# Performance work log

Hardware: AMD Instinct MI355X
Metric: run time of the kernel (lower is better)

## Reference

```python
import jax, jax.numpy as jnp
import numpy as np

N_ENT, E, M, STEPS, B, H, C = 500000, 128, 8, 3, 4096, 256, 16

def setup_inputs() -> dict:
    key = jax.random.key(0)
    ks = jax.random.split(key, 13)
    s = 0.05
    return {
        "entity_ids": jax.random.randint(ks[0], (B, STEPS + 1), 0, N_ENT),
        "module_ids": jax.random.randint(ks[1], (B, STEPS), 0, M),
        "embedding": jax.random.normal(ks[2], (N_ENT, E), jnp.float32),
        "W_in": jax.random.normal(ks[3], (M, E, E), jnp.float32) * s,
        "b_in": jax.random.normal(ks[4], (M, E), jnp.float32) * s,
        "W_bias": jax.random.normal(ks[5], (M, E, E), jnp.float32) * s,
        "b_bias": jax.random.normal(ks[6], (M, E), jnp.float32) * s,
        "W_f": jax.random.normal(ks[7], (M, 2 * E, E), jnp.float32) * s,
        "b_f": jax.random.normal(ks[8], (M, E), jnp.float32) * s,
        "W1": jax.random.normal(ks[9], (E, H), jnp.float32) * s,
        "b1": jax.random.normal(ks[10], (H,), jnp.float32) * s,
        "W2": jax.random.normal(ks[11], (H, C), jnp.float32) * s,
        "b2": jax.random.normal(ks[12], (C,), jnp.float32) * s,
    }

def reference(entity_ids, module_ids, embedding, W_in, b_in, W_bias, b_bias,
              W_f, b_f, W1, b1, W2, b2):
    # x: [B, E] embedding of each path's start entity
    x = embedding[entity_ids[:, 0]]

    def step(x, inputs):
        mid, eid = inputs                      # [B], [B]
        bias = embedding[eid]                  # [B, E]
        h_in = jax.nn.relu(jnp.einsum('be,beo->bo', x, W_in[mid]) + b_in[mid])
        h_bi = jax.nn.relu(jnp.einsum('be,beo->bo', bias, W_bias[mid]) + b_bias[mid])
        h = jnp.concatenate([h_in, h_bi], axis=1)  # [B, 2E]
        x_new = jnp.tanh(jnp.einsum('bf,bfo->bo', h, W_f[mid]) + b_f[mid])
        return x_new, None

    xs = (module_ids.T, entity_ids[:, 1:].T)   # [STEPS, B] each
    x, _ = jax.lax.scan(step, x, xs)

    # classifier: Linear -> ReLU -> Linear
    h = jax.nn.relu(x @ W1 + b1)
    return h @ W2 + b2
```

## Files before the change

### kernel.cpp

```cpp
#include <hip/hip_runtime.h>

#define BB      4096
#define EE      128
#define MM      8
#define NSTEPS  3
#define HH      256
#define CC      16

#define TS      16
#define NBMAX   (BB/TS + MM)
#define HT      17
#define FB      1024

#define NFRAGBLK 1096

typedef __attribute__((ext_vector_type(8))) short  bf16x8;
typedef __attribute__((ext_vector_type(4))) float  f32x4;

__device__ __forceinline__ unsigned short bf16_rn(float v) {
    unsigned u = __float_as_uint(v);
    return (unsigned short)((u + 0x7FFFu + ((u >> 16) & 1u)) >> 16);
}
__device__ __forceinline__ float bf16_f(unsigned short h) {
    return __uint_as_float(((unsigned)h) << 16);
}
__device__ __forceinline__ void split8(const float* v, bf16x8& hi, bf16x8& lo) {
    #pragma unroll
    for (int i = 0; i < 8; i++) {
        unsigned short h = bf16_rn(v[i]);
        hi[i] = (short)h;
        lo[i] = (short)bf16_rn(v[i] - bf16_f(h));
    }
}
#define MFMA(a,b,c) __builtin_amdgcn_mfma_f32_16x16x32_bf16((a),(b),(c),0,0,0)
__device__ __forceinline__ f32x4 mfma3(bf16x8 ah, bf16x8 al, bf16x8 bh, bf16x8 bl, f32x4 c) {
    c = MFMA(ah, bh, c);
    c = MFMA(ah, bl, c);
    c = MFMA(al, bh, c);
    return c;
}

__global__ __launch_bounds__(256) void convert_kernel(
    const float* __restrict__ W_in, const float* __restrict__ W_bias,
    const float* __restrict__ W_f,  const float* __restrict__ W1,
    const float* __restrict__ W2,   unsigned short* __restrict__ wf)
{
    const int b = blockIdx.x, tid = threadIdx.x;
    unsigned short* dhi = wf + (size_t)b * FB;
    unsigned short* dlo = dhi + 512;
    #pragma unroll
    for (int half = 0; half < 2; half++) {
        const int el = tid + half * 256;
        const int ln = el >> 3, j = el & 7;
        const int krel = ((ln >> 4) << 3) + j;
        const int nrel = ln & 15;
        float v;
        if (b < 512) {
            const int bb = b & 255;
            const int kc = bb & 3, nt = (bb >> 2) & 7, m = bb >> 5;
            const float* src = (b < 256 ? W_in : W_bias) + (size_t)m * EE * EE;
            v = src[(size_t)(kc*32 + krel) * EE + nt*16 + nrel];
        } else if (b < 1024) {
            const int bb = b - 512;
            const int kc = bb & 7, nt = (bb >> 3) & 7, m = bb >> 6;
            v = W_f[(size_t)m * 2*EE*EE + (size_t)(kc*32 + krel) * EE + nt*16 + nrel];
        } else if (b < 1088) {
            const int bb = b - 1024;
            const int kc = bb & 3, nt = bb >> 2;
            v = W1[(size_t)(kc*32 + krel) * HH + nt*16 + nrel];
        } else {
            const int kc = b - 1088;
            v = W2[(size_t)(kc*32 + krel) * CC + nrel];
        }
        const unsigned short h = bf16_rn(v);
        dhi[el] = h;
        dlo[el] = bf16_rn(v - bf16_f(h));
    }
}

__global__ __launch_bounds__(1024) void prep_kernel(
    const int* __restrict__ module_ids,
    int* __restrict__ blockMod,
    int* __restrict__ perm)
{
    __shared__ int waveCnt [16][NSTEPS][MM];
    __shared__ int waveBase[16][NSTEPS][MM];
    __shared__ int cursor  [16][NSTEPS][MM];
    __shared__ int base        [NSTEPS][MM];
    const int tid  = threadIdx.x;
    const int wid  = tid >> 6;
    const int lane = tid & 63;

    if (tid < 16*NSTEPS*MM) (&waveCnt[0][0][0])[tid] = 0;
    for (int i = tid; i < NSTEPS*NBMAX*TS; i += 1024) perm[i] = -1;
    __syncthreads();

    for (int t = 0; t < NSTEPS; t++) {
        #pragma unroll
        for (int c = 0; c < 4; c++) {
            const int s = (wid << 8) + (c << 6) + lane;
            const int m = module_ids[s*NSTEPS + t];
            unsigned long long bal[MM];
            #pragma unroll
            for (int k = 0; k < MM; k++) bal[k] = __ballot(m == k);
            if (lane < MM) waveCnt[wid][t][lane] += __popcll(bal[lane]);
        }
    }
    __syncthreads();

    if (tid < NSTEPS) {
        const int t = tid;
        int blk = 0;
        for (int m = 0; m < MM; m++) {
            int tot = 0;
            for (int w = 0; w < 16; w++) { waveBase[w][t][m] = tot; tot += waveCnt[w][t][m]; }
            base[t][m] = blk * TS;
            const int nb = (tot + TS - 1) / TS;
            for (int b = 0; b < nb; b++) blockMod[t*NBMAX + blk + b] = m;
            blk += nb;
        }
        for (; blk < NBMAX; blk++) blockMod[t*NBMAX + blk] = -1;
    }
    __syncthreads();

    if (tid < 16*NSTEPS*MM) {
        const int w = tid / (NSTEPS*MM), r = tid % (NSTEPS*MM), t = r / MM, m = r % MM;
        cursor[w][t][m] = base[t][m] + waveBase[w][t][m];
    }
    __syncthreads();

    for (int t = 0; t < NSTEPS; t++) {
        #pragma unroll
        for (int c = 0; c < 4; c++) {
            const int s = (wid << 8) + (c << 6) + lane;
            const int m = module_ids[s*NSTEPS + t];
            unsigned long long bal[MM];
            #pragma unroll
            for (int k = 0; k < MM; k++) bal[k] = __ballot(m == k);
            const unsigned long long below = (1ull << lane) - 1ull;
            const int rank = __popcll(bal[m] & below);
            perm[t*NBMAX*TS + cursor[wid][t][m] + rank] = s;
            if (lane < MM) cursor[wid][t][lane] += __popcll(bal[lane]);
        }
    }
}

__global__ __launch_bounds__(256) void step_kernel(
    const int t,
    const int*   __restrict__ entity_ids,
    const float* __restrict__ embedding,
    const float* __restrict__ b_in, const float* __restrict__ b_bias,
    const float* __restrict__ b_f,
    const unsigned short* __restrict__ wf,
    const int*   __restrict__ blockMod,
    const int*   __restrict__ perm,
    float* __restrict__ xbuf)
{
    const int bid = blockIdx.x;
    const int m = blockMod[t*NBMAX + bid];
    if (m < 0) return;
    const int tid  = threadIdx.x;
    const int lane = tid & 63, wave = tid >> 6;
    const int row16 = lane & 15, quad = lane >> 4;
    const int pb = (t*NBMAX + bid)*TS;

    __shared__ float hs[2*EE][HT];

    const int sA = perm[pb + row16];
    int sSt[4];
    #pragma unroll
    for (int r = 0; r < 4; r++) sSt[r] = perm[pb + quad*4 + r];
    const int sAc = sA < 0 ? 0 : sA;

    const float* xrow;
    if (t == 0) {
        const int e0 = entity_ids[sAc*(NSTEPS+1)];
        xrow = embedding + (size_t)e0*EE;
    } else {
        xrow = xbuf + (size_t)sAc*EE;
    }
    const int e1 = entity_ids[sAc*(NSTEPS+1) + t + 1];
    const float* brow = embedding + (size_t)e1*EE;

    bf16x8 xh[4], xl[4], eh[4], el_[4];
    #pragma unroll
    for (int kc = 0; kc < 4; kc++) {
        const int off = kc*32 + quad*8;
        float vv[8];
        *(float4*)(vv)     = *(const float4*)(xrow + off);
        *(float4*)(vv + 4) = *(const float4*)(xrow + off + 4);
        split8(vv, xh[kc], xl[kc]);
        *(float4*)(vv)     = *(const float4*)(brow + off);
        *(float4*)(vv + 4) = *(const float4*)(brow + off + 4);
        split8(vv, eh[kc], el_[kc]);
    }

    f32x4 aci[2] = {{0.f,0.f,0.f,0.f},{0.f,0.f,0.f,0.f}};
    f32x4 acb[2] = {{0.f,0.f,0.f,0.f},{0.f,0.f,0.f,0.f}};
    #pragma unroll
    for (int i = 0; i < 2; i++) {
        const int nt = wave + 4*i;
        #pragma unroll
        for (int kc = 0; kc < 4; kc++) {
            const unsigned short* bI = wf + (size_t)((m*8 + nt)*4 + kc)*FB;
            const unsigned short* bB = wf + (size_t)(256 + (m*8 + nt)*4 + kc)*FB;
            const bf16x8 wih = *(const bf16x8*)(bI + lane*8);
            const bf16x8 wil = *(const bf16x8*)(bI + 512 + lane*8);
            const bf16x8 wbh = *(const bf16x8*)(bB + lane*8);
            const bf16x8 wbl = *(const bf16x8*)(bB + 512 + lane*8);
            aci[i] = mfma3(xh[kc], xl[kc], wih, wil, aci[i]);
            acb[i] = mfma3(eh[kc], el_[kc], wbh, wbl, acb[i]);
        }
    }

    #pragma unroll
    for (int i = 0; i < 2; i++) {
        const int col = (wave + 4*i)*16 + row16;
        const float bin = b_in [m*EE + col];
        const float bbi = b_bias[m*EE + col];
        #pragma unroll
        for (int r = 0; r < 4; r++) {
            hs[col][quad*4 + r]      = fmaxf(aci[i][r] + bin, 0.f);
            hs[EE + col][quad*4 + r] = fmaxf(acb[i][r] + bbi, 0.f);
        }
    }
    __syncthreads();

    f32x4 acf[2] = {{0.f,0.f,0.f,0.f},{0.f,0.f,0.f,0.f}};
    #pragma unroll
    for (int kc = 0; kc < 8; kc++) {
        float vv[8];
        #pragma unroll
        for (int j = 0; j < 8; j++) vv[j] = hs[kc*32 + quad*8 + j][row16];
        bf16x8 ah, al;
        split8(vv, ah, al);
        #pragma unroll
        for (int i = 0; i < 2; i++) {
            const int nt = wave + 4*i;
            const unsigned short* bF = wf + (size_t)(512 + (m*8 + nt)*8 + kc)*FB;
            const bf16x8 wfh = *(const bf16x8*)(bF + lane*8);
            const bf16x8 wfl = *(const bf16x8*)(bF + 512 + lane*8);
            acf[i] = mfma3(ah, al, wfh, wfl, acf[i]);
        }
    }
    #pragma unroll
    for (int i = 0; i < 2; i++) {
        const int col = (wave + 4*i)*16 + row16;
        const float bfv = b_f[m*EE + col];
        #pragma unroll
        for (int r = 0; r < 4; r++) {
            const int s = sSt[r];
            if (s >= 0) xbuf[(size_t)s*EE + col] = tanhf(acf[i][r] + bfv);
        }
    }
}

__global__ __launch_bounds__(256) void final_kernel(
    const float* __restrict__ xbuf,
    const float* __restrict__ b1v, const float* __restrict__ b2,
    const unsigned short* __restrict__ wf,
    float* __restrict__ out)
{
    const int tid = threadIdx.x, bid = blockIdx.x;
    const int lane = tid & 63, wave = tid >> 6;
    const int row16 = lane & 15, quad = lane >> 4;
    const int sbase = bid * TS;

    __shared__ float hs[HH][HT];
    __shared__ float red[4][TS][CC];

    const float* xrow = xbuf + (size_t)(sbase + row16)*EE;
    bf16x8 xh[4], xl[4];
    #pragma unroll
    for (int kc = 0; kc < 4; kc++) {
        const int off = kc*32 + quad*8;
        float vv[8];
        *(float4*)(vv)     = *(const float4*)(xrow + off);
        *(float4*)(vv + 4) = *(const float4*)(xrow + off + 4);
        split8(vv, xh[kc], xl[kc]);
    }

    f32x4 a1[4] = {{0.f,0.f,0.f,0.f},{0.f,0.f,0.f,0.f},{0.f,0.f,0.f,0.f},{0.f,0.f,0.f,0.f}};
    #pragma unroll
    for (int i = 0; i < 4; i++) {
        const int nt = wave + 4*i;
        #pragma unroll
        for (int kc = 0; kc < 4; kc++) {
            const unsigned short* bW = wf + (size_t)(1024 + nt*4 + kc)*FB;
            const bf16x8 wh = *(const bf16x8*)(bW + lane*8);
            const bf16x8 wl = *(const bf16x8*)(bW + 512 + lane*8);
            a1[i] = mfma3(xh[kc], xl[kc], wh, wl, a1[i]);
        }
    }
    #pragma unroll
    for (int i = 0; i < 4; i++) {
        const int col = (wave + 4*i)*16 + row16;
        const float b = b1v[col];
        #pragma unroll
        for (int r = 0; r < 4; r++)
            hs[col][quad*4 + r] = fmaxf(a1[i][r] + b, 0.f);
    }
    __syncthreads();

    f32x4 a2 = {0.f,0.f,0.f,0.f};
    #pragma unroll
    for (int u = 0; u < 2; u++) {
        const int kc = wave*2 + u;
        float vv[8];
        #pragma unroll
        for (int j = 0; j < 8; j++) vv[j] = hs[kc*32 + quad*8 + j][row16];
        bf16x8 ah, al;
        split8(vv, ah, al);
        const unsigned short* bW = wf + (size_t)(1088 + kc)*FB;
        const bf16x8 wh = *(const bf16x8*)(bW + lane*8);
        const bf16x8 wl = *(const bf16x8*)(bW + 512 + lane*8);
        a2 = mfma3(ah, al, wh, wl, a2);
    }
    #pragma unroll
    for (int r = 0; r < 4; r++) red[wave][quad*4 + r][row16] = a2[r];
    __syncthreads();

    {
        const int s = tid >> 4, c = tid & 15;
        const float v = red[0][s][c] + red[1][s][c] + red[2][s][c] + red[3][s][c] + b2[c];
        out[(size_t)(sbase + s)*CC + c] = v;
    }
}

extern "C" void kernel_launch(void* const* d_in, const int* in_sizes, int n_in,
                              void* d_out, int out_size, void* d_ws, size_t ws_size,
                              hipStream_t stream) {
    const int*   entity_ids = (const int*)  d_in[0];
    const int*   module_ids = (const int*)  d_in[1];
    const float* embedding  = (const float*)d_in[2];
    const float* W_in   = (const float*)d_in[3];
    const float* b_in   = (const float*)d_in[4];
    const float* W_bias = (const float*)d_in[5];
    const float* b_bias = (const float*)d_in[6];
    const float* W_f    = (const float*)d_in[7];
    const float* b_f    = (const float*)d_in[8];
    const float* W1     = (const float*)d_in[9];
    const float* b1     = (const float*)d_in[10];
    const float* W2     = (const float*)d_in[11];
    const float* b2     = (const float*)d_in[12];
    float* out = (float*)d_out;

    int* blockMod = (int*)d_ws;
    int* perm     = blockMod + 1024;
    float* xbuf   = (float*)(blockMod + 1024 + NSTEPS*NBMAX*TS);
    unsigned short* wfb = (unsigned short*)(xbuf + (size_t)BB*EE);

    convert_kernel<<<NFRAGBLK, 256, 0, stream>>>(W_in, W_bias, W_f, W1, W2, wfb);
    prep_kernel<<<1, 1024, 0, stream>>>(module_ids, blockMod, perm);
    for (int t = 0; t < NSTEPS; t++) {
        step_kernel<<<NBMAX, 256, 0, stream>>>(t, entity_ids, embedding,
                                               b_in, b_bias, b_f,
                                               wfb, blockMod, perm, xbuf);
    }
    final_kernel<<<BB/TS, 256, 0, stream>>>(xbuf, b1, b2, wfb, out);
}
```

Baseline: 377.0 us.

## Pre-split embeddings to bf16 pairs, parallelize routing prep, widen step blocks

Embedding rows for every step are gathered and split into bf16 hi/lo pairs up front, inside the weight-conversion launch. The state x is stored as bf16 hi/lo instead of fp32, and hidden activations are written to shared memory already in MFMA fragment layout, so the per-step float splits and the transposed shared-memory reads go away. The single-block prep kernel becomes a parallel count pass, a one-block plan and a 48-block scatter. Step and final kernels move to 512 threads with one output tile per wave. In exchange there are more launches and more workspace traffic for the pre-split embeddings.

```diff
diff --git a/kernel.cpp b/kernel.cpp
--- a/kernel.cpp
+++ b/kernel.cpp
@@ -9,10 +9,13 @@
 
 #define TS      16
 #define NBMAX   (BB/TS + MM)
-#define HT      17
 #define FB      1024
 
 #define NFRAGBLK 1096
+
+#define ECONV0   1096
+#define COUNT0   2120
+#define GRID1    2168
 
 typedef __attribute__((ext_vector_type(8))) short  bf16x8;
 typedef __attribute__((ext_vector_type(4))) float  f32x4;
@@ -31,6 +34,10 @@
         hi[i] = (short)h;
         lo[i] = (short)bf16_rn(v[i] - bf16_f(h));
     }
+}
+__device__ __forceinline__ void split1(float v, unsigned short& h, unsigned short& l) {
+    h = bf16_rn(v);
+    l = bf16_rn(v - bf16_f(h));
 }
 #define MFMA(a,b,c) __builtin_amdgcn_mfma_f32_16x16x32_bf16((a),(b),(c),0,0,0)
 __device__ __forceinline__ f32x4 mfma3(bf16x8 ah, bf16x8 al, bf16x8 bh, bf16x8 bl, f32x4 c) {
@@ -41,120 +48,153 @@
 }
 
 __global__ __launch_bounds__(256) void convert_kernel(
+    const int*   __restrict__ entity_ids, const int* __restrict__ module_ids,
+    const float* __restrict__ embedding,
     const float* __restrict__ W_in, const float* __restrict__ W_bias,
     const float* __restrict__ W_f,  const float* __restrict__ W1,
-    const float* __restrict__ W2,   unsigned short* __restrict__ wf)
+    const float* __restrict__ W2,
+    unsigned short* __restrict__ wf,
+    unsigned short* __restrict__ x0h, unsigned short* __restrict__ x0l,
+    unsigned short* __restrict__ ebh, unsigned short* __restrict__ ebl,
+    int* __restrict__ wcnt)
 {
     const int b = blockIdx.x, tid = threadIdx.x;
-    unsigned short* dhi = wf + (size_t)b * FB;
-    unsigned short* dlo = dhi + 512;
-    #pragma unroll
-    for (int half = 0; half < 2; half++) {
-        const int el = tid + half * 256;
-        const int ln = el >> 3, j = el & 7;
-        const int krel = ((ln >> 4) << 3) + j;
-        const int nrel = ln & 15;
-        float v;
-        if (b < 512) {
-            const int bb = b & 255;
-            const int kc = bb & 3, nt = (bb >> 2) & 7, m = bb >> 5;
-            const float* src = (b < 256 ? W_in : W_bias) + (size_t)m * EE * EE;
-            v = src[(size_t)(kc*32 + krel) * EE + nt*16 + nrel];
-        } else if (b < 1024) {
-            const int bb = b - 512;
-            const int kc = bb & 7, nt = (bb >> 3) & 7, m = bb >> 6;
-            v = W_f[(size_t)m * 2*EE*EE + (size_t)(kc*32 + krel) * EE + nt*16 + nrel];
-        } else if (b < 1088) {
-            const int bb = b - 1024;
-            const int kc = bb & 3, nt = bb >> 2;
-            v = W1[(size_t)(kc*32 + krel) * HH + nt*16 + nrel];
-        } else {
-            const int kc = b - 1088;
-            v = W2[(size_t)(kc*32 + krel) * CC + nrel];
-        }
-        const unsigned short h = bf16_rn(v);
-        dhi[el] = h;
-        dlo[el] = bf16_rn(v - bf16_f(h));
-    }
-}
-
-__global__ __launch_bounds__(1024) void prep_kernel(
-    const int* __restrict__ module_ids,
+    if (b < NFRAGBLK) {
+        unsigned short* dhi = wf + (size_t)b * FB;
+        unsigned short* dlo = dhi + 512;
+        #pragma unroll
+        for (int half = 0; half < 2; half++) {
+            const int el = tid + half * 256;
+            const int ln = el >> 3, j = el & 7;
+            const int krel = ((ln >> 4) << 3) + j;
+            const int nrel = ln & 15;
+            float v;
+            if (b < 512) {
+                const int bb = b & 255;
+                const int kc = bb & 3, nt = (bb >> 2) & 7, m = bb >> 5;
+                const float* src = (b < 256 ? W_in : W_bias) + (size_t)m * EE * EE;
+                v = src[(size_t)(kc*32 + krel) * EE + nt*16 + nrel];
+            } else if (b < 1024) {
+                const int bb = b - 512;
+                const int kc = bb & 7, nt = (bb >> 3) & 7, m = bb >> 6;
+                v = W_f[(size_t)m * 2*EE*EE + (size_t)(kc*32 + krel) * EE + nt*16 + nrel];
+            } else if (b < 1088) {
+                const int bb = b - 1024;
+                const int kc = bb & 3, nt = bb >> 2;
+                v = W1[(size_t)(kc*32 + krel) * HH + nt*16 + nrel];
+            } else {
+                const int kc = b - 1088;
+                v = W2[(size_t)(kc*32 + krel) * CC + nrel];
+            }
+            split1(v, dhi[el], dlo[el]);
+        }
+    } else if (b < COUNT0) {
+        const int u = b - ECONV0;
+        const int g = u >> 8, wb = u & 255;
+        const int rloc = tid >> 4, cpart = tid & 15;
+        const int s = wb*16 + rloc;
+        const int eid = entity_ids[s*(NSTEPS+1) + g];
+        const float* src = embedding + (size_t)eid*EE + cpart*8;
+        float vv[8];
+        *(float4*)(vv)     = *(const float4*)(src);
+        *(float4*)(vv + 4) = *(const float4*)(src + 4);
+        bf16x8 hi, lo;
+        split8(vv, hi, lo);
+        unsigned short* dh = (g == 0 ? x0h : ebh + (size_t)(g-1)*BB*EE) + (size_t)s*EE + cpart*8;
+        unsigned short* dl = (g == 0 ? x0l : ebl + (size_t)(g-1)*BB*EE) + (size_t)s*EE + cpart*8;
+        *(bf16x8*)dh = hi;
+        *(bf16x8*)dl = lo;
+    } else {
+        const int u = b - COUNT0;
+        const int t = u >> 4, chunk = u & 15;
+        const int wave = tid >> 6, lane = tid & 63;
+        const int s = chunk*256 + wave*64 + lane;
+        const int m = module_ids[s*NSTEPS + t];
+        unsigned long long bal[MM];
+        #pragma unroll
+        for (int k = 0; k < MM; k++) bal[k] = __ballot(m == k);
+        if (lane < MM)
+            wcnt[((t*16 + chunk)*4 + wave)*MM + lane] = __popcll(bal[lane]);
+    }
+}
+
+__global__ __launch_bounds__(256) void plan_kernel(
+    const int* __restrict__ wcnt,
     int* __restrict__ blockMod,
+    int* __restrict__ gbase,
     int* __restrict__ perm)
 {
-    __shared__ int waveCnt [16][NSTEPS][MM];
-    __shared__ int waveBase[16][NSTEPS][MM];
-    __shared__ int cursor  [16][NSTEPS][MM];
-    __shared__ int base        [NSTEPS][MM];
-    const int tid  = threadIdx.x;
-    const int wid  = tid >> 6;
-    const int lane = tid & 63;
-
-    if (tid < 16*NSTEPS*MM) (&waveCnt[0][0][0])[tid] = 0;
-    for (int i = tid; i < NSTEPS*NBMAX*TS; i += 1024) perm[i] = -1;
-    __syncthreads();
-
-    for (int t = 0; t < NSTEPS; t++) {
-        #pragma unroll
-        for (int c = 0; c < 4; c++) {
-            const int s = (wid << 8) + (c << 6) + lane;
-            const int m = module_ids[s*NSTEPS + t];
-            unsigned long long bal[MM];
-            #pragma unroll
-            for (int k = 0; k < MM; k++) bal[k] = __ballot(m == k);
-            if (lane < MM) waveCnt[wid][t][lane] += __popcll(bal[lane]);
-        }
-    }
-    __syncthreads();
-
+    __shared__ int scnt[NSTEPS*16*4*MM];
+    __shared__ int tot [NSTEPS][MM];
+    __shared__ int base[NSTEPS][MM];
+    const int tid = threadIdx.x;
+
+    for (int i = tid; i < NSTEPS*16*4*MM; i += 256) scnt[i] = wcnt[i];
+    for (int i = tid; i < NSTEPS*NBMAX*TS; i += 256) perm[i] = -1;
+    __syncthreads();
+
+    if (tid < NSTEPS*MM) {
+        const int t = tid / MM, m = tid % MM;
+        int s = 0;
+        for (int sl = 0; sl < 64; sl++) s += scnt[(t*64 + sl)*MM + m];
+        tot[t][m] = s;
+    }
+    __syncthreads();
     if (tid < NSTEPS) {
         const int t = tid;
         int blk = 0;
         for (int m = 0; m < MM; m++) {
-            int tot = 0;
-            for (int w = 0; w < 16; w++) { waveBase[w][t][m] = tot; tot += waveCnt[w][t][m]; }
             base[t][m] = blk * TS;
-            const int nb = (tot + TS - 1) / TS;
+            const int nb = (tot[t][m] + TS - 1) / TS;
             for (int b = 0; b < nb; b++) blockMod[t*NBMAX + blk + b] = m;
             blk += nb;
         }
         for (; blk < NBMAX; blk++) blockMod[t*NBMAX + blk] = -1;
     }
     __syncthreads();
-
-    if (tid < 16*NSTEPS*MM) {
-        const int w = tid / (NSTEPS*MM), r = tid % (NSTEPS*MM), t = r / MM, m = r % MM;
-        cursor[w][t][m] = base[t][m] + waveBase[w][t][m];
-    }
-    __syncthreads();
-
-    for (int t = 0; t < NSTEPS; t++) {
-        #pragma unroll
-        for (int c = 0; c < 4; c++) {
-            const int s = (wid << 8) + (c << 6) + lane;
-            const int m = module_ids[s*NSTEPS + t];
-            unsigned long long bal[MM];
-            #pragma unroll
-            for (int k = 0; k < MM; k++) bal[k] = __ballot(m == k);
-            const unsigned long long below = (1ull << lane) - 1ull;
-            const int rank = __popcll(bal[m] & below);
-            perm[t*NBMAX*TS + cursor[wid][t][m] + rank] = s;
-            if (lane < MM) cursor[wid][t][lane] += __popcll(bal[lane]);
-        }
-    }
-}
-
-__global__ __launch_bounds__(256) void step_kernel(
+    if (tid < NSTEPS*MM) {
+        const int t = tid / MM, m = tid % MM;
+        int run = base[t][m];
+        for (int sl = 0; sl < 64; sl++) {
+            const int idx = (t*64 + sl)*MM + m;
+            gbase[idx] = run;
+            run += scnt[idx];
+        }
+    }
+}
+
+__global__ __launch_bounds__(256) void scatter_kernel(
+    const int* __restrict__ module_ids,
+    const int* __restrict__ gbase,
+    int* __restrict__ perm)
+{
+    const int u = blockIdx.x;
+    const int t = u >> 4, chunk = u & 15;
+    const int tid = threadIdx.x, wave = tid >> 6, lane = tid & 63;
+    __shared__ int gb[4*MM];
+    if (tid < 4*MM) gb[tid] = gbase[((t*16 + chunk)*4)*MM + tid];
+    __syncthreads();
+
+    const int s = chunk*256 + wave*64 + lane;
+    const int m = module_ids[s*NSTEPS + t];
+    unsigned long long bal[MM];
+    #pragma unroll
+    for (int k = 0; k < MM; k++) bal[k] = __ballot(m == k);
+    const unsigned long long below = (1ull << lane) - 1ull;
+    const int rank = __popcll(bal[m] & below);
+    perm[t*NBMAX*TS + gb[wave*MM + m] + rank] = s;
+}
+
+__global__ __launch_bounds__(512) void step_kernel(
     const int t,
-    const int*   __restrict__ entity_ids,
-    const float* __restrict__ embedding,
+    const unsigned short* __restrict__ x0h, const unsigned short* __restrict__ x0l,
+    const unsigned short* __restrict__ ebh, const unsigned short* __restrict__ ebl,
     const float* __restrict__ b_in, const float* __restrict__ b_bias,
     const float* __restrict__ b_f,
     const unsigned short* __restrict__ wf,
     const int*   __restrict__ blockMod,
     const int*   __restrict__ perm,
-    float* __restrict__ xbuf)
+    unsigned short* __restrict__ xsh, unsigned short* __restrict__ xsl)
 {
     const int bid = blockIdx.x;
     const int m = blockMod[t*NBMAX + bid];
@@ -164,99 +204,96 @@
     const int row16 = lane & 15, quad = lane >> 4;
     const int pb = (t*NBMAX + bid)*TS;
 
-    __shared__ float hs[2*EE][HT];
-
-    const int sA = perm[pb + row16];
-    int sSt[4];
-    #pragma unroll
-    for (int r = 0; r < 4; r++) sSt[r] = perm[pb + quad*4 + r];
+    __shared__ __align__(16) unsigned short hfh[8][512];
+    __shared__ __align__(16) unsigned short hfl[8][512];
+    __shared__ int sids[TS];
+
+    if (tid < TS) sids[tid] = perm[pb + tid];
+    __syncthreads();
+
+    const int sA  = sids[row16];
     const int sAc = sA < 0 ? 0 : sA;
 
-    const float* xrow;
-    if (t == 0) {
-        const int e0 = entity_ids[sAc*(NSTEPS+1)];
-        xrow = embedding + (size_t)e0*EE;
-    } else {
-        xrow = xbuf + (size_t)sAc*EE;
-    }
-    const int e1 = entity_ids[sAc*(NSTEPS+1) + t + 1];
-    const float* brow = embedding + (size_t)e1*EE;
+    const unsigned short* xh_p = (t == 0 ? x0h : xsh) + (size_t)sAc*EE;
+    const unsigned short* xl_p = (t == 0 ? x0l : xsl) + (size_t)sAc*EE;
+    const unsigned short* eh_p = ebh + (size_t)t*BB*EE + (size_t)sAc*EE;
+    const unsigned short* el_p = ebl + (size_t)t*BB*EE + (size_t)sAc*EE;
 
     bf16x8 xh[4], xl[4], eh[4], el_[4];
     #pragma unroll
     for (int kc = 0; kc < 4; kc++) {
         const int off = kc*32 + quad*8;
-        float vv[8];
-        *(float4*)(vv)     = *(const float4*)(xrow + off);
-        *(float4*)(vv + 4) = *(const float4*)(xrow + off + 4);
-        split8(vv, xh[kc], xl[kc]);
-        *(float4*)(vv)     = *(const float4*)(brow + off);
-        *(float4*)(vv + 4) = *(const float4*)(brow + off + 4);
-        split8(vv, eh[kc], el_[kc]);
-    }
-
-    f32x4 aci[2] = {{0.f,0.f,0.f,0.f},{0.f,0.f,0.f,0.f}};
-    f32x4 acb[2] = {{0.f,0.f,0.f,0.f},{0.f,0.f,0.f,0.f}};
-    #pragma unroll
-    for (int i = 0; i < 2; i++) {
-        const int nt = wave + 4*i;
-        #pragma unroll
-        for (int kc = 0; kc < 4; kc++) {
-            const unsigned short* bI = wf + (size_t)((m*8 + nt)*4 + kc)*FB;
-            const unsigned short* bB = wf + (size_t)(256 + (m*8 + nt)*4 + kc)*FB;
-            const bf16x8 wih = *(const bf16x8*)(bI + lane*8);
-            const bf16x8 wil = *(const bf16x8*)(bI + 512 + lane*8);
-            const bf16x8 wbh = *(const bf16x8*)(bB + lane*8);
-            const bf16x8 wbl = *(const bf16x8*)(bB + 512 + lane*8);
-            aci[i] = mfma3(xh[kc], xl[kc], wih, wil, aci[i]);
-            acb[i] = mfma3(eh[kc], el_[kc], wbh, wbl, acb[i]);
-        }
-    }
-
-    #pragma unroll
-    for (int i = 0; i < 2; i++) {
-        const int col = (wave + 4*i)*16 + row16;
+        xh[kc]  = *(const bf16x8*)(xh_p + off);
+        xl[kc]  = *(const bf16x8*)(xl_p + off);
+        eh[kc]  = *(const bf16x8*)(eh_p + off);
+        el_[kc] = *(const bf16x8*)(el_p + off);
+    }
+
+    f32x4 aci = {0.f,0.f,0.f,0.f}, acb = {0.f,0.f,0.f,0.f};
+    #pragma unroll
+    for (int kc = 0; kc < 4; kc++) {
+        const unsigned short* bI = wf + (size_t)((m*8 + wave)*4 + kc)*FB;
+        const unsigned short* bB = wf + (size_t)(256 + (m*8 + wave)*4 + kc)*FB;
+        const bf16x8 wih = *(const bf16x8*)(bI + lane*8);
+        const bf16x8 wil = *(const bf16x8*)(bI + 512 + lane*8);
+        const bf16x8 wbh = *(const bf16x8*)(bB + lane*8);
+        const bf16x8 wbl = *(const bf16x8*)(bB + 512 + lane*8);
+        aci = mfma3(xh[kc], xl[kc], wih, wil, aci);
+        acb = mfma3(eh[kc], el_[kc], wbh, wbl, acb);
+    }
+
+    {
+        const int col = wave*16 + row16;
         const float bin = b_in [m*EE + col];
         const float bbi = b_bias[m*EE + col];
         #pragma unroll
         for (int r = 0; r < 4; r++) {
-            hs[col][quad*4 + r]      = fmaxf(aci[i][r] + bin, 0.f);
-            hs[EE + col][quad*4 + r] = fmaxf(acb[i][r] + bbi, 0.f);
-        }
-    }
-    __syncthreads();
-
-    f32x4 acf[2] = {{0.f,0.f,0.f,0.f},{0.f,0.f,0.f,0.f}};
+            const int row = quad*4 + r;
+            {
+                const float v = fmaxf(aci[r] + bin, 0.f);
+                const int k = col, kc = k >> 5;
+                const int idx = (row + 16*((k >> 3) & 3))*8 + (k & 7);
+                split1(v, hfh[kc][idx], hfl[kc][idx]);
+            }
+            {
+                const float v = fmaxf(acb[r] + bbi, 0.f);
+                const int k = EE + col, kc = k >> 5;
+                const int idx = (row + 16*((k >> 3) & 3))*8 + (k & 7);
+                split1(v, hfh[kc][idx], hfl[kc][idx]);
+            }
+        }
+    }
+    __syncthreads();
+
+    f32x4 acf = {0.f,0.f,0.f,0.f};
     #pragma unroll
     for (int kc = 0; kc < 8; kc++) {
-        float vv[8];
-        #pragma unroll
-        for (int j = 0; j < 8; j++) vv[j] = hs[kc*32 + quad*8 + j][row16];
-        bf16x8 ah, al;
-        split8(vv, ah, al);
-        #pragma unroll
-        for (int i = 0; i < 2; i++) {
-            const int nt = wave + 4*i;
-            const unsigned short* bF = wf + (size_t)(512 + (m*8 + nt)*8 + kc)*FB;
-            const bf16x8 wfh = *(const bf16x8*)(bF + lane*8);
-            const bf16x8 wfl = *(const bf16x8*)(bF + 512 + lane*8);
-            acf[i] = mfma3(ah, al, wfh, wfl, acf[i]);
-        }
-    }
-    #pragma unroll
-    for (int i = 0; i < 2; i++) {
-        const int col = (wave + 4*i)*16 + row16;
+        const bf16x8 ah = *(const bf16x8*)(&hfh[kc][lane*8]);
+        const bf16x8 al = *(const bf16x8*)(&hfl[kc][lane*8]);
+        const unsigned short* bF = wf + (size_t)(512 + (m*8 + wave)*8 + kc)*FB;
+        const bf16x8 wfh = *(const bf16x8*)(bF + lane*8);
+        const bf16x8 wfl = *(const bf16x8*)(bF + 512 + lane*8);
+        acf = mfma3(ah, al, wfh, wfl, acf);
+    }
+    {
+        const int col = wave*16 + row16;
         const float bfv = b_f[m*EE + col];
         #pragma unroll
         for (int r = 0; r < 4; r++) {
-            const int s = sSt[r];
-            if (s >= 0) xbuf[(size_t)s*EE + col] = tanhf(acf[i][r] + bfv);
-        }
-    }
-}
-
-__global__ __launch_bounds__(256) void final_kernel(
-    const float* __restrict__ xbuf,
+            const int s = sids[quad*4 + r];
+            if (s >= 0) {
+                const float v = tanhf(acf[r] + bfv);
+                unsigned short h, l;
+                split1(v, h, l);
+                xsh[(size_t)s*EE + col] = h;
+                xsl[(size_t)s*EE + col] = l;
+            }
+        }
+    }
+}
+
+__global__ __launch_bounds__(512) void final_kernel(
+    const unsigned short* __restrict__ xsh, const unsigned short* __restrict__ xsl,
     const float* __restrict__ b1v, const float* __restrict__ b2,
     const unsigned short* __restrict__ wf,
     float* __restrict__ out)
@@ -266,24 +303,24 @@
     const int row16 = lane & 15, quad = lane >> 4;
     const int sbase = bid * TS;
 
-    __shared__ float hs[HH][HT];
-    __shared__ float red[4][TS][CC];
-
-    const float* xrow = xbuf + (size_t)(sbase + row16)*EE;
+    __shared__ __align__(16) unsigned short hfh[8][512];
+    __shared__ __align__(16) unsigned short hfl[8][512];
+    __shared__ float red[8][TS][CC];
+
+    const unsigned short* xh_p = xsh + (size_t)(sbase + row16)*EE;
+    const unsigned short* xl_p = xsl + (size_t)(sbase + row16)*EE;
     bf16x8 xh[4], xl[4];
     #pragma unroll
     for (int kc = 0; kc < 4; kc++) {
         const int off = kc*32 + quad*8;
-        float vv[8];
-        *(float4*)(vv)     = *(const float4*)(xrow + off);
-        *(float4*)(vv + 4) = *(const float4*)(xrow + off + 4);
-        split8(vv, xh[kc], xl[kc]);
-    }
-
-    f32x4 a1[4] = {{0.f,0.f,0.f,0.f},{0.f,0.f,0.f,0.f},{0.f,0.f,0.f,0.f},{0.f,0.f,0.f,0.f}};
-    #pragma unroll
-    for (int i = 0; i < 4; i++) {
-        const int nt = wave + 4*i;
+        xh[kc] = *(const bf16x8*)(xh_p + off);
+        xl[kc] = *(const bf16x8*)(xl_p + off);
+    }
+
+    f32x4 a1[2] = {{0.f,0.f,0.f,0.f},{0.f,0.f,0.f,0.f}};
+    #pragma unroll
+    for (int i = 0; i < 2; i++) {
+        const int nt = wave + 8*i;
         #pragma unroll
         for (int kc = 0; kc < 4; kc++) {
             const unsigned short* bW = wf + (size_t)(1024 + nt*4 + kc)*FB;
@@ -293,24 +330,25 @@
         }
     }
     #pragma unroll
-    for (int i = 0; i < 4; i++) {
-        const int col = (wave + 4*i)*16 + row16;
+    for (int i = 0; i < 2; i++) {
+        const int col = (wave + 8*i)*16 + row16;
         const float b = b1v[col];
         #pragma unroll
-        for (int r = 0; r < 4; r++)
-            hs[col][quad*4 + r] = fmaxf(a1[i][r] + b, 0.f);
+        for (int r = 0; r < 4; r++) {
+            const int row = quad*4 + r;
+            const float v = fmaxf(a1[i][r] + b, 0.f);
+            const int kc = col >> 5;
+            const int idx = (row + 16*((col >> 3) & 3))*8 + (col & 7);
+            split1(v, hfh[kc][idx], hfl[kc][idx]);
+        }
     }
     __syncthreads();
 
     f32x4 a2 = {0.f,0.f,0.f,0.f};
-    #pragma unroll
-    for (int u = 0; u < 2; u++) {
-        const int kc = wave*2 + u;
-        float vv[8];
-        #pragma unroll
-        for (int j = 0; j < 8; j++) vv[j] = hs[kc*32 + quad*8 + j][row16];
-        bf16x8 ah, al;
-        split8(vv, ah, al);
+    {
+        const int kc = wave;
+        const bf16x8 ah = *(const bf16x8*)(&hfh[kc][lane*8]);
+        const bf16x8 al = *(const bf16x8*)(&hfl[kc][lane*8]);
         const unsigned short* bW = wf + (size_t)(1088 + kc)*FB;
         const bf16x8 wh = *(const bf16x8*)(bW + lane*8);
         const bf16x8 wl = *(const bf16x8*)(bW + 512 + lane*8);
@@ -320,9 +358,11 @@
     for (int r = 0; r < 4; r++) red[wave][quad*4 + r][row16] = a2[r];
     __syncthreads();
 
-    {
+    if (tid < TS*CC) {
         const int s = tid >> 4, c = tid & 15;
-        const float v = red[0][s][c] + red[1][s][c] + red[2][s][c] + red[3][s][c] + b2[c];
+        float v = b2[c];
+        #pragma unroll
+        for (int w = 0; w < 8; w++) v += red[w][s][c];
         out[(size_t)(sbase + s)*CC + c] = v;
     }
 }
@@ -345,17 +385,28 @@
     const float* b2     = (const float*)d_in[12];
     float* out = (float*)d_out;
 
-    int* blockMod = (int*)d_ws;
-    int* perm     = blockMod + 1024;
-    float* xbuf   = (float*)(blockMod + 1024 + NSTEPS*NBMAX*TS);
-    unsigned short* wfb = (unsigned short*)(xbuf + (size_t)BB*EE);
-
-    convert_kernel<<<NFRAGBLK, 256, 0, stream>>>(W_in, W_bias, W_f, W1, W2, wfb);
-    prep_kernel<<<1, 1024, 0, stream>>>(module_ids, blockMod, perm);
+    char* ws = (char*)d_ws;
+    int* blockMod = (int*)(ws + 0);
+    int* perm     = (int*)(ws + 4096);
+    int* wcnt     = (int*)(ws + 54784);
+    int* gbase    = (int*)(ws + 60928);
+    unsigned short* wfb = (unsigned short*)(ws + 131072);
+    unsigned short* x0h = (unsigned short*)(ws + (4u<<20));
+    unsigned short* x0l = (unsigned short*)(ws + (5u<<20));
+    unsigned short* xsh = (unsigned short*)(ws + (6u<<20));
+    unsigned short* xsl = (unsigned short*)(ws + (7u<<20));
+    unsigned short* ebh = (unsigned short*)(ws + (8u<<20));
+    unsigned short* ebl = (unsigned short*)(ws + (11u<<20));
+
+    convert_kernel<<<GRID1, 256, 0, stream>>>(entity_ids, module_ids, embedding,
+                                              W_in, W_bias, W_f, W1, W2,
+                                              wfb, x0h, x0l, ebh, ebl, wcnt);
+    plan_kernel<<<1, 256, 0, stream>>>(wcnt, blockMod, gbase, perm);
+    scatter_kernel<<<48, 256, 0, stream>>>(module_ids, gbase, perm);
     for (int t = 0; t < NSTEPS; t++) {
-        step_kernel<<<NBMAX, 256, 0, stream>>>(t, entity_ids, embedding,
+        step_kernel<<<NBMAX, 512, 0, stream>>>(t, x0h, x0l, ebh, ebl,
                                                b_in, b_bias, b_f,
-                                               wfb, blockMod, perm, xbuf);
-    }
-    final_kernel<<<BB/TS, 256, 0, stream>>>(xbuf, b1, b2, wfb, out);
-}
+                                               wfb, blockMod, perm, xsh, xsl);
+    }
+    final_kernel<<<BB/TS, 512, 0, stream>>>(xsh, xsl, b1, b2, wfb, out);
+}
```

New measurement: 368.6 us. 2.2% less time.
